# Optimization experiments

Measured on AMD Instinct MI355X. Metric: run time of the kernel, lower is better.

The kernel has to match this reference:

```python
import jax, jax.numpy as jnp
import numpy as np

T, B, E = 48, 16, 512
V, S, G = 50000, 40000, 32
K_VAL, NUM_C = 8, 20


def setup_inputs() -> dict:
    key = jax.random.key(0)
    ks = jax.random.split(key, 5)
    return {
        "word_embeddings": jax.random.normal(ks[0], (T, B, E), jnp.float32),
        "prev_word_embeddings": jax.random.normal(ks[1], (T, B, E), jnp.float32),
        "location_context": jnp.zeros((T, B, E), jnp.float32),
        "logits_globals": jax.random.normal(ks[2], (T * B, V), jnp.float32),
        "SC": jax.random.normal(ks[3], (S, E), jnp.float32),
        "neighbours_table": jax.random.randint(ks[4], (V, G), 0, S, jnp.int32),
        "K": K_VAL,
        "num_C": NUM_C,
    }


def reference(word_embeddings, prev_word_embeddings, location_context,
              logits_globals, SC, neighbours_table, K, num_C):
    T_, B_, E_ = word_embeddings.shape
    S_ = SC.shape[0]
    G_ = neighbours_table.shape[1]

    # --- update_context_average: sliding-window (box-filter) sum via cumsum ---
    cat = jnp.concatenate([prev_word_embeddings, word_embeddings], axis=0)  # [2T,B,E]
    cs = jnp.cumsum(cat, axis=0)
    win = cs[T_:2 * T_] - cs[T_ - num_C:2 * T_ - num_C]
    loc_ctx = location_context + win / num_C                                 # [T,B,E]

    # --- top-K globals -> padded sense-neighbour gather ---
    _, topk = jax.lax.top_k(logits_globals, K)                               # [T*B,K]
    neigh = neighbours_table[topk]                                           # [T*B,K,G]
    all_sense_neighbours = neigh.reshape(T_, B_, K * G_)                     # [T,B,KG]
    senses_context = SC[all_sense_neighbours]                                # [T,B,KG,E]

    # --- cosine similarity (torch.nn.CosineSimilarity, eps=1e-8) ---
    eps = 1e-8
    a = loc_ctx[:, :, None, :]                                               # [T,B,1,E]
    an = jnp.maximum(jnp.linalg.norm(a, axis=-1), eps)
    bn = jnp.maximum(jnp.linalg.norm(senses_context, axis=-1), eps)
    cos = jnp.sum(a * senses_context, axis=-1) / (an * bn)                   # [T,B,KG]

    # --- pick best sense, scatter into epsilon-softmax ---
    first_idx = jnp.argmax(cos, axis=2)                                      # [T,B]
    first_sense = jnp.take_along_axis(
        all_sense_neighbours, first_idx[:, :, None], axis=2)[:, :, 0]        # [T,B]
    chosen = 1.0 - eps * (S_ - 1)
    sm = jnp.full((T_, B_, S_), eps, jnp.float32)
    tt = jnp.arange(T_)[:, None]
    bb = jnp.arange(B_)[None, :]
    sm = sm.at[tt, bb, first_sense].set(chosen)
    predictions_senses = jnp.log(sm).reshape(T_ * B_, S_)

    predictions_globals = jax.nn.log_softmax(logits_globals, axis=1)
    return predictions_globals, predictions_senses
```

## Files before the change

kernel.cpp:

```cpp
#include <hip/hip_runtime.h>
#include <cstdint>
#include <cmath>

#define T_ 48
#define B_ 16
#define E_ 512
#define V_ 50000
#define S_ 40000
#define G_ 32
#define K_ 8
#define NUMC 20
#define ROWS (T_*B_)
#define V4 (V_/4)
#define E4 (E_/4)
#define NCAND 4096

typedef float floatx4 __attribute__((ext_vector_type(4)));

__global__ __launch_bounds__(512) void k_topk_lse_lsm(const float* __restrict__ logits,
                                                      int* __restrict__ topk,
                                                      float* __restrict__ out_g) {
    __shared__ float smax[512];
    __shared__ float wm[8], ws[8];
    __shared__ float cand_v[NCAND];
    __shared__ int   cand_i[NCAND];
    __shared__ int   ncand;
    __shared__ float s_tau, s_lse;

    int row = blockIdx.x;
    int tid = threadIdx.x;
    int lane = tid & 63, w = tid >> 6;
    const float4* rp = (const float4*)(logits + (size_t)row * V_);
    const float L2E = 1.4426950408889634f;

    float v8[8]; int i8[8];
    #pragma unroll
    for (int j = 0; j < 8; ++j) { v8[j] = -INFINITY; i8[j] = 0x7fffffff; }
    float m = -INFINITY, s = 0.f;

    for (int it = tid; it < V4; it += 512) {
        float4 v = rp[it];
        float xs[4] = {v.x, v.y, v.z, v.w};
        #pragma unroll
        for (int c = 0; c < 4; ++c) {
            float x = xs[c];
            if (x > v8[7]) {
                v8[7] = x; i8[7] = it * 4 + c;
                #pragma unroll
                for (int k = 7; k >= 1; --k) {
                    bool sw = v8[k] > v8[k-1];
                    float tv = sw ? v8[k-1] : v8[k];
                    int   ti = sw ? i8[k-1] : i8[k];
                    v8[k-1] = sw ? v8[k] : v8[k-1];
                    i8[k-1] = sw ? i8[k] : i8[k-1];
                    v8[k] = tv; i8[k] = ti;
                }
            }
            if (x > m) { s *= __builtin_exp2f((m - x) * L2E); m = x; }
            s += __builtin_exp2f((x - m) * L2E);
        }
    }
    smax[tid] = m;

    float mm = m, sacc = s;
    #pragma unroll
    for (int off = 32; off; off >>= 1) {
        float om = __shfl_down(mm, off);
        float os = __shfl_down(sacc, off);
        float M = fmaxf(mm, om);
        sacc = sacc * __builtin_exp2f((mm - M) * L2E) + os * __builtin_exp2f((om - M) * L2E);
        mm = M;
    }
    if (lane == 0) { wm[w] = mm; ws[w] = sacc; }
    if (tid == 0) ncand = 0;
    __syncthreads();

    if (tid < 64) {
        float t8[8];
        #pragma unroll
        for (int j = 0; j < 8; ++j) t8[j] = smax[tid * 8 + j];
        #pragma unroll
        for (int r = 0; r < 8; ++r) {
            float lm = t8[0];
            #pragma unroll
            for (int j = 1; j < 8; ++j) lm = fmaxf(lm, t8[j]);
            #pragma unroll
            for (int mask = 1; mask < 64; mask <<= 1)
                lm = fmaxf(lm, __shfl_xor(lm, mask));
            if (tid == 0 && r == 7) s_tau = lm;
            #pragma unroll
            for (int j = 0; j < 8; ++j) if (t8[j] == lm) t8[j] = -INFINITY;
        }
        if (tid == 0) {
            float M = wm[0];
            #pragma unroll
            for (int i = 1; i < 8; ++i) M = fmaxf(M, wm[i]);
            float S = 0.f;
            #pragma unroll
            for (int i = 0; i < 8; ++i) S += ws[i] * __builtin_exp2f((wm[i] - M) * L2E);
            s_lse = M + logf(S);
        }
    }
    __syncthreads();

    float tau = s_tau;
    #pragma unroll
    for (int j = 0; j < 8; ++j) {
        if (v8[j] >= tau) {
            int p = atomicAdd(&ncand, 1);
            if (p < NCAND) { cand_v[p] = v8[j]; cand_i[p] = i8[j]; }
        }
    }
    __syncthreads();

    if (tid < 64) {
        int C = ncand; if (C > NCAND) C = NCAND;
        for (int r = 0; r < 8; ++r) {
            float bv = -INFINITY; int bi = 0x7fffffff;
            for (int c = tid; c < C; c += 64) {
                float v = cand_v[c]; int i = cand_i[c];
                if (v > bv || (v == bv && i < bi)) { bv = v; bi = i; }
            }
            #pragma unroll
            for (int mask = 1; mask < 64; mask <<= 1) {
                float ov = __shfl_xor(bv, mask);
                int   oi = __shfl_xor(bi, mask);
                if (ov > bv || (ov == bv && oi < bi)) { bv = ov; bi = oi; }
            }
            if (tid == 0) topk[row * K_ + r] = bi;
            for (int c = tid; c < C; c += 64)
                if (cand_i[c] == bi) { cand_v[c] = -INFINITY; cand_i[c] = 0x7fffffff; }
        }
    }

    float l = s_lse;
    floatx4* og = (floatx4*)(out_g + (size_t)row * V_);
    for (int it = tid; it < V4; it += 512) {
        float4 v = rp[it];
        floatx4 o = {v.x - l, v.y - l, v.z - l, v.w - l};
        __builtin_nontemporal_store(o, og + it);
    }
}

__global__ __launch_bounds__(512) void k_sense(const float* __restrict__ word,
                                               const float* __restrict__ prev,
                                               const float* __restrict__ locc,
                                               const int* __restrict__ topk,
                                               const int* __restrict__ neigh,
                                               const float* __restrict__ SC,
                                               float* __restrict__ outS,
                                               float log_eps, float log_chosen) {
    __shared__ __align__(16) float a[E_];
    __shared__ int   sidx[K_ * G_];
    __shared__ float warr[8];
    __shared__ float wbv[8];
    __shared__ int   wbn[8];
    __shared__ float a_n;

    int row = blockIdx.x;
    int t = row / B_, b = row % B_;
    int tid = threadIdx.x;
    int lane = tid & 63, w = tid >> 6;

    float acc = 0.f;
    #pragma unroll
    for (int d = 0; d < NUMC; ++d) {
        int src = t - d;
        const float* p = (src >= 0) ? (word + (size_t)(src * B_ + b) * E_)
                                    : (prev + (size_t)((T_ + src) * B_ + b) * E_);
        acc += p[tid];
    }
    float a0 = locc[(size_t)row * E_ + tid] + acc / (float)NUMC;
    a[tid] = a0;
    if (tid < K_ * G_)
        sidx[tid] = neigh[(size_t)topk[row * K_ + (tid >> 5)] * G_ + (tid & 31)];

    floatx4 fv = {log_eps, log_eps, log_eps, log_eps};
    floatx4* orow = (floatx4*)(outS + (size_t)row * S_);
    for (int i = tid; i < S_ / 4; i += 512)
        __builtin_nontemporal_store(fv, orow + i);

    float pp = a0 * a0;
    #pragma unroll
    for (int off = 32; off; off >>= 1) pp += __shfl_down(pp, off);
    if (lane == 0) warr[w] = pp;
    __syncthreads();
    if (tid == 0) {
        float tt = warr[0];
        #pragma unroll
        for (int i = 1; i < 8; ++i) tt += warr[i];
        a_n = fmaxf(sqrtf(tt), 1e-8f);
    }
    __syncthreads();

    const float4* a4 = (const float4*)a;
    float4 aA = a4[lane], aB = a4[lane + 64];
    float an = a_n;

    float best = -INFINITY; int bn = 0x7fffffff;
    for (int n = w; n < K_ * G_; n += 16) {
        int n2 = n + 8;
        const float4* sp0 = (const float4*)(SC + (size_t)sidx[n]  * E_);
        const float4* sp1 = (const float4*)(SC + (size_t)sidx[n2] * E_);
        float4 s0A = sp0[lane], s0B = sp0[lane + 64];
        float4 s1A = sp1[lane], s1B = sp1[lane + 64];
        float dot0 = s0A.x * aA.x + s0A.y * aA.y + s0A.z * aA.z + s0A.w * aA.w
                   + s0B.x * aB.x + s0B.y * aB.y + s0B.z * aB.z + s0B.w * aB.w;
        float nr0  = s0A.x * s0A.x + s0A.y * s0A.y + s0A.z * s0A.z + s0A.w * s0A.w
                   + s0B.x * s0B.x + s0B.y * s0B.y + s0B.z * s0B.z + s0B.w * s0B.w;
        float dot1 = s1A.x * aA.x + s1A.y * aA.y + s1A.z * aA.z + s1A.w * aA.w
                   + s1B.x * aB.x + s1B.y * aB.y + s1B.z * aB.z + s1B.w * aB.w;
        float nr1  = s1A.x * s1A.x + s1A.y * s1A.y + s1A.z * s1A.z + s1A.w * s1A.w
                   + s1B.x * s1B.x + s1B.y * s1B.y + s1B.z * s1B.z + s1B.w * s1B.w;
        #pragma unroll
        for (int off = 32; off; off >>= 1) {
            dot0 += __shfl_down(dot0, off);
            nr0  += __shfl_down(nr0,  off);
            dot1 += __shfl_down(dot1, off);
            nr1  += __shfl_down(nr1,  off);
        }
        if (lane == 0) {
            float cs0 = dot0 / (an * fmaxf(sqrtf(nr0), 1e-8f));
            if (cs0 > best) { best = cs0; bn = n; }
            float cs1 = dot1 / (an * fmaxf(sqrtf(nr1), 1e-8f));
            if (cs1 > best) { best = cs1; bn = n2; }
        }
    }
    if (lane == 0) { wbv[w] = best; wbn[w] = bn; }
    __syncthreads();
    if (tid == 0) {
        float bv = wbv[0]; int bnn = wbn[0];
        #pragma unroll
        for (int i = 1; i < 8; ++i) {
            if (wbv[i] > bv || (wbv[i] == bv && wbn[i] < bnn)) { bv = wbv[i]; bnn = wbn[i]; }
        }
        outS[(size_t)row * S_ + sidx[bnn]] = log_chosen;
    }
}

extern "C" void kernel_launch(void* const* d_in, const int* in_sizes, int n_in,
                              void* d_out, int out_size, void* d_ws, size_t ws_size,
                              hipStream_t stream) {
    const float* word   = (const float*)d_in[0];
    const float* prev   = (const float*)d_in[1];
    const float* locc   = (const float*)d_in[2];
    const float* logits = (const float*)d_in[3];
    const float* SC     = (const float*)d_in[4];
    const int*   neigh  = (const int*)d_in[5];

    float* out_g = (float*)d_out;
    float* out_s = out_g + (size_t)ROWS * V_;

    int* topk = (int*)d_ws;

    k_topk_lse_lsm<<<ROWS, 512, 0, stream>>>(logits, topk, out_g);

    float log_eps    = logf(1e-8f);
    float log_chosen = logf(1.0f - 1e-8f * (float)(S_ - 1));
    k_sense<<<ROWS, 512, 0, stream>>>(word, prev, locc, topk, neigh, SC,
                                      out_s, log_eps, log_chosen);
}
```

Measured before the change: 628.4 us.

## Split top-k pass into max prepass then threshold filter; move fill to separate kernel

The top-k/logsumexp kernel now reads each logits row twice. A first pass computes per-thread maxima, which yield the row max and an 8th-largest-per-thread threshold. A second pass accumulates exp sums against the known max and appends elements above the threshold to a shared candidate list, which removes the per-element insertion sort and the online-softmax rescaling. The log-epsilon fill of the senses output moves out of k_sense into a separate grid-stride kernel launched first. This costs an extra read of logits and an extra launch, and the candidate buffer is reduced to 1024 entries, which risks overflow if many values tie at the threshold.

```diff
diff --git a/kernel.cpp b/kernel.cpp
--- a/kernel.cpp
+++ b/kernel.cpp
@@ -13,7 +13,7 @@
 #define ROWS (T_*B_)
 #define V4 (V_/4)
 #define E4 (E_/4)
-#define NCAND 4096
+#define NCAND 1024
 
 typedef float floatx4 __attribute__((ext_vector_type(4)));
 
@@ -21,11 +21,11 @@
                                                       int* __restrict__ topk,
                                                       float* __restrict__ out_g) {
     __shared__ float smax[512];
-    __shared__ float wm[8], ws[8];
+    __shared__ float ssum[8];
     __shared__ float cand_v[NCAND];
     __shared__ int   cand_i[NCAND];
     __shared__ int   ncand;
-    __shared__ float s_tau, s_lse;
+    __shared__ float s_m, s_tau, s_lse;
 
     int row = blockIdx.x;
     int tid = threadIdx.x;
@@ -33,83 +33,65 @@
     const float4* rp = (const float4*)(logits + (size_t)row * V_);
     const float L2E = 1.4426950408889634f;
 
-    float v8[8]; int i8[8];
-    #pragma unroll
-    for (int j = 0; j < 8; ++j) { v8[j] = -INFINITY; i8[j] = 0x7fffffff; }
-    float m = -INFINITY, s = 0.f;
-
+    float m = -INFINITY;
+    for (int it = tid; it < V4; it += 512) {
+        float4 v = rp[it];
+        m = fmaxf(m, fmaxf(fmaxf(v.x, v.y), fmaxf(v.z, v.w)));
+    }
+    smax[tid] = m;
+    if (tid == 0) ncand = 0;
+    __syncthreads();
+
+    if (tid < 64) {
+        float t8[8];
+        #pragma unroll
+        for (int j = 0; j < 8; ++j) t8[j] = smax[tid * 8 + j];
+        #pragma unroll
+        for (int r = 0; r < 8; ++r) {
+            float lm = t8[0];
+            #pragma unroll
+            for (int j = 1; j < 8; ++j) lm = fmaxf(lm, t8[j]);
+            #pragma unroll
+            for (int mask = 1; mask < 64; mask <<= 1)
+                lm = fmaxf(lm, __shfl_xor(lm, mask));
+            if (tid == 0) {
+                if (r == 0) s_m = lm;
+                if (r == 7) s_tau = lm;
+            }
+            #pragma unroll
+            for (int j = 0; j < 8; ++j) if (t8[j] == lm) t8[j] = -INFINITY;
+        }
+    }
+    __syncthreads();
+
+    float rm  = s_m;
+    float tau = s_tau;
+    float nml2 = -rm * L2E;
+
+    float sum = 0.f;
     for (int it = tid; it < V4; it += 512) {
         float4 v = rp[it];
         float xs[4] = {v.x, v.y, v.z, v.w};
         #pragma unroll
         for (int c = 0; c < 4; ++c) {
             float x = xs[c];
-            if (x > v8[7]) {
-                v8[7] = x; i8[7] = it * 4 + c;
-                #pragma unroll
-                for (int k = 7; k >= 1; --k) {
-                    bool sw = v8[k] > v8[k-1];
-                    float tv = sw ? v8[k-1] : v8[k];
-                    int   ti = sw ? i8[k-1] : i8[k];
-                    v8[k-1] = sw ? v8[k] : v8[k-1];
-                    i8[k-1] = sw ? i8[k] : i8[k-1];
-                    v8[k] = tv; i8[k] = ti;
-                }
-            }
-            if (x > m) { s *= __builtin_exp2f((m - x) * L2E); m = x; }
-            s += __builtin_exp2f((x - m) * L2E);
-        }
-    }
-    smax[tid] = m;
-
-    float mm = m, sacc = s;
+            sum += __builtin_exp2f(__builtin_fmaf(x, L2E, nml2));
+            if (x >= tau) {
+                int p = atomicAdd(&ncand, 1);
+                if (p < NCAND) { cand_v[p] = x; cand_i[p] = it * 4 + c; }
+            }
+        }
+    }
     #pragma unroll
-    for (int off = 32; off; off >>= 1) {
-        float om = __shfl_down(mm, off);
-        float os = __shfl_down(sacc, off);
-        float M = fmaxf(mm, om);
-        sacc = sacc * __builtin_exp2f((mm - M) * L2E) + os * __builtin_exp2f((om - M) * L2E);
-        mm = M;
-    }
-    if (lane == 0) { wm[w] = mm; ws[w] = sacc; }
-    if (tid == 0) ncand = 0;
-    __syncthreads();
-
-    if (tid < 64) {
-        float t8[8];
-        #pragma unroll
-        for (int j = 0; j < 8; ++j) t8[j] = smax[tid * 8 + j];
-        #pragma unroll
-        for (int r = 0; r < 8; ++r) {
-            float lm = t8[0];
-            #pragma unroll
-            for (int j = 1; j < 8; ++j) lm = fmaxf(lm, t8[j]);
-            #pragma unroll
-            for (int mask = 1; mask < 64; mask <<= 1)
-                lm = fmaxf(lm, __shfl_xor(lm, mask));
-            if (tid == 0 && r == 7) s_tau = lm;
-            #pragma unroll
-            for (int j = 0; j < 8; ++j) if (t8[j] == lm) t8[j] = -INFINITY;
-        }
-        if (tid == 0) {
-            float M = wm[0];
-            #pragma unroll
-            for (int i = 1; i < 8; ++i) M = fmaxf(M, wm[i]);
-            float S = 0.f;
-            #pragma unroll
-            for (int i = 0; i < 8; ++i) S += ws[i] * __builtin_exp2f((wm[i] - M) * L2E);
-            s_lse = M + logf(S);
-        }
-    }
-    __syncthreads();
-
-    float tau = s_tau;
-    #pragma unroll
-    for (int j = 0; j < 8; ++j) {
-        if (v8[j] >= tau) {
-            int p = atomicAdd(&ncand, 1);
-            if (p < NCAND) { cand_v[p] = v8[j]; cand_i[p] = i8[j]; }
-        }
+    for (int off = 32; off; off >>= 1) sum += __shfl_down(sum, off);
+    if (lane == 0) ssum[w] = sum;
+    __syncthreads();
+
+    if (tid == 0) {
+        float tot = ssum[0];
+        #pragma unroll
+        for (int i = 1; i < 8; ++i) tot += ssum[i];
+        s_lse = rm + logf(tot);
     }
     __syncthreads();
 
@@ -142,6 +124,13 @@
     }
 }
 
+__global__ __launch_bounds__(256) void k_fill(float4* __restrict__ out, float val, int n4) {
+    int i = blockIdx.x * 256 + threadIdx.x;
+    int stride = gridDim.x * 256;
+    float4 v = make_float4(val, val, val, val);
+    for (; i < n4; i += stride) out[i] = v;
+}
+
 __global__ __launch_bounds__(512) void k_sense(const float* __restrict__ word,
                                                const float* __restrict__ prev,
                                                const float* __restrict__ locc,
@@ -149,7 +138,7 @@
                                                const int* __restrict__ neigh,
                                                const float* __restrict__ SC,
                                                float* __restrict__ outS,
-                                               float log_eps, float log_chosen) {
+                                               float log_chosen) {
     __shared__ __align__(16) float a[E_];
     __shared__ int   sidx[K_ * G_];
     __shared__ float warr[8];
@@ -174,11 +163,6 @@
     a[tid] = a0;
     if (tid < K_ * G_)
         sidx[tid] = neigh[(size_t)topk[row * K_ + (tid >> 5)] * G_ + (tid & 31)];
-
-    floatx4 fv = {log_eps, log_eps, log_eps, log_eps};
-    floatx4* orow = (floatx4*)(outS + (size_t)row * S_);
-    for (int i = tid; i < S_ / 4; i += 512)
-        __builtin_nontemporal_store(fv, orow + i);
 
     float pp = a0 * a0;
     #pragma unroll
@@ -253,10 +237,12 @@
 
     int* topk = (int*)d_ws;
 
+    float log_eps = logf(1e-8f);
+    k_fill<<<2048, 256, 0, stream>>>((float4*)out_s, log_eps, ROWS * (S_ / 4));
+
     k_topk_lse_lsm<<<ROWS, 512, 0, stream>>>(logits, topk, out_g);
 
-    float log_eps    = logf(1e-8f);
     float log_chosen = logf(1.0f - 1e-8f * (float)(S_ - 1));
     k_sense<<<ROWS, 512, 0, stream>>>(word, prev, locc, topk, neigh, SC,
-                                      out_s, log_eps, log_chosen);
-}
+                                      out_s, log_chosen);
+}
```

Result: faster. 525.6 us (-16.4%).
